# Kernel tuning notes

Hardware: AMD Instinct MI355X
Metric: run time of the kernel (lower is better)

Reference implementation:

```python
import jax, jax.numpy as jnp
import numpy as np

THRESHOLD = 10.0  # degrees, PlanetaryGraphConstruction default


def _norm_adj(lon):
    # lon: [B, P] longitudes in degrees
    diff = jnp.abs(lon[:, :, None] - lon[:, None, :]) % 360.0
    dist = jnp.minimum(diff, 360.0 - diff)            # circular angular distance, diag = 0
    mask = (dist < THRESHOLD).astype(lon.dtype)       # distance edges (diag included: 0 < 10)
    P = lon.shape[1]
    A = mask + jnp.eye(P, dtype=lon.dtype)            # GCNConv add_self_loops appends another self loop
    deg = A.sum(-1)
    dinv = jax.lax.rsqrt(jnp.maximum(deg, 1e-12))
    return A * dinv[:, :, None] * dinv[:, None, :]    # D^-1/2 (A+I) D^-1/2, [B, P, P]


def setup_inputs() -> dict:
    key = jax.random.key(0)
    ks = jax.random.split(key, 10)
    B, P, Din, H, Dout = 65536, 12, 32, 128, 3
    L = 3
    x = jax.random.uniform(ks[0], (B, P, Din), dtype=jnp.float32) * 360.0  # col 0 = longitude in degrees
    s = 0.02
    return {
        "x": x,
        "W_in": jax.random.normal(ks[1], (Din, H), jnp.float32) * s,
        "b_in": jnp.zeros((H,), jnp.float32),
        "W_gcn": jax.random.normal(ks[2], (L, H, H), jnp.float32) * s,
        "b_gcn": jnp.zeros((L, H), jnp.float32),
        "W_out1": jax.random.normal(ks[3], (H, H // 2), jnp.float32) * s,
        "b_out1": jnp.zeros((H // 2,), jnp.float32),
        "W_out2": jax.random.normal(ks[4], (H // 2, Dout), jnp.float32) * s,
        "b_out2": jnp.zeros((Dout,), jnp.float32),
    }


def reference(x, W_in, b_in, W_gcn, b_gcn, W_out1, b_out1, W_out2, b_out2):
    # x: [B, P, Din]
    Ahat = _norm_adj(x[:, :, 0])                      # [B, P, P] normalized adjacency
    h = x @ W_in + b_in                               # input projection, [B, P, H]
    for l in range(W_gcn.shape[0]):                   # GCN layers (dropout = identity in eval)
        h = jnp.einsum('bij,bjh->bih', Ahat, h @ W_gcn[l]) + b_gcn[l]
        h = jax.nn.relu(h)
    g = h.mean(axis=1)                                # mean pool over planets, [B, H]
    g = jax.nn.relu(g @ W_out1 + b_out1)
    return g @ W_out2 + b_out2                        # [B, Dout]
```

## Files before the change

kernel.cpp:

```cpp
#include <hip/hip_runtime.h>


typedef _Float16 half4v __attribute__((ext_vector_type(4)));
typedef _Float16 half8v __attribute__((ext_vector_type(8)));
typedef float    float4v __attribute__((ext_vector_type(4)));

constexpr int PP = 12, DIN = 32, H = 128, HO = 64, DOUT = 3, NL = 3;
constexpr int NB = 8;
constexpr int AP2 = 72;
constexpr int GTS = 136;

constexpr int WS_WG = 4096, WS_W1 = 53248, WS_TOT = 61440;

__global__ __launch_bounds__(256)
void prep_weights(const float* __restrict__ W_in, const float* __restrict__ W_gcn,
                  const float* __restrict__ W_out1, _Float16* __restrict__ ws)
{
    int e = blockIdx.x * 256 + threadIdx.x;
    if (e < WS_WG) {
        int n = e >> 5, k = e & 31;
        ws[e] = (_Float16)W_in[k * H + n];
    } else if (e < WS_W1) {
        int e2 = e - WS_WG;
        int l = e2 >> 14, r = e2 & 16383, n = r >> 7, k = r & 127;
        ws[e] = (_Float16)W_gcn[l * (H * H) + k * H + n];
    } else if (e < WS_TOT) {
        int e3 = e - WS_W1;
        int o = e3 >> 7, k = e3 & 127;
        ws[e] = (_Float16)W_out1[k * HO + o];
    }
}

__device__ inline half4v pk4(float a, float b, float c, float d) {
    half4v r; r[0] = (_Float16)a; r[1] = (_Float16)b; r[2] = (_Float16)c; r[3] = (_Float16)d;
    return r;
}

__global__ __launch_bounds__(256, 4)
void gnn_mfma(const float* __restrict__ x,
              const float* __restrict__ b_in,
              const float* __restrict__ b_gcn,
              const float* __restrict__ b_out1,
              const float* __restrict__ W_out2,
              const float* __restrict__ b_out2,
              const _Float16* __restrict__ ws,
              float* __restrict__ out)
{
    __shared__ __align__(16) _Float16 hf[2][12][512];
    _Float16* Am  = &hf[0][0][0];
    _Float16* gTT = &hf[0][0][0];
    float*    psf = (float*)&hf[1][0][0];

    const int tid  = threadIdx.x;
    const int lane = tid & 63, wave = tid >> 6;
    const int q = lane >> 4, qm = lane & 15;
    const int hh = lane >> 5, l32 = lane & 31;
    const int b0 = blockIdx.x * NB;
    const float* xblk = x + (size_t)b0 * (PP * DIN);
    const _Float16* WgT = ws + WS_WG;

    float lon_own = 0.f;
    if (l32 < PP) lon_own = xblk[(hh * 48 + wave * PP + l32) * DIN];
    float4 xa[3], xb[3];
    #pragma unroll
    for (int nt = 0; nt < 3; ++nt) {
        const float* p = xblk + (16 * nt + qm) * DIN + 8 * q;
        xa[nt] = *(const float4*)p;
        xb[nt] = *(const float4*)(p + 4);
    }

    {
        float lonj[PP];
        #pragma unroll
        for (int j = 0; j < PP; ++j) lonj[j] = __shfl(lon_own, j, 32);
        float deg = 1.0f;
        #pragma unroll
        for (int j = 0; j < PP; ++j) {
            float d = fabsf(lon_own - lonj[j]);
            d = fminf(d, 360.0f - d);
            deg += (d < 10.0f) ? 1.0f : 0.0f;
        }
        float dinv_own = rsqrtf(fmaxf(deg, 1e-12f));
        float dj[PP];
        #pragma unroll
        for (int j = 0; j < PP; ++j) dj[j] = __shfl(dinv_own, j, 32);

        if (l32 < PP) {
            _Float16* Ar = Am + (hh * 48 + wave * PP + l32) * AP2;
            half8v z = {0, 0, 0, 0, 0, 0, 0, 0};
            #pragma unroll
            for (int c = 0; c < 48; c += 8) *(half8v*)&Ar[c] = z;
            _Float16 vals[PP];
            #pragma unroll
            for (int j = 0; j < PP; ++j) {
                float d = fabsf(lon_own - lonj[j]);
                d = fminf(d, 360.0f - d);
                float a = (d < 10.0f) ? 1.0f : 0.0f;
                if (j == l32) a += 1.0f;
                vals[j] = (_Float16)(a * dinv_own * dj[j]);
            }
            #pragma unroll
            for (int t4 = 0; t4 < 3; ++t4) {
                half4v v;
                v[0] = vals[4 * t4]; v[1] = vals[4 * t4 + 1];
                v[2] = vals[4 * t4 + 2]; v[3] = vals[4 * t4 + 3];
                *(half4v*)&Ar[wave * PP + 4 * t4] = v;
            }
        }
    }
    __syncthreads();

    half4v bAf[2][7];
    #pragma unroll
    for (int h = 0; h < 2; ++h) {
        const _Float16* Ah = Am + h * 48 * AP2;
        bAf[h][0] = *(const half4v*)&Ah[qm * AP2 + 4 * q];
        bAf[h][1] = *(const half4v*)&Ah[qm * AP2 + 16 + 4 * q];
        bAf[h][2] = *(const half4v*)&Ah[(16 + qm) * AP2 + 4 * q];
        bAf[h][3] = *(const half4v*)&Ah[(16 + qm) * AP2 + 16 + 4 * q];
        bAf[h][4] = *(const half4v*)&Ah[(16 + qm) * AP2 + 32 + 4 * q];
        bAf[h][5] = *(const half4v*)&Ah[(32 + qm) * AP2 + 16 + 4 * q];
        bAf[h][6] = *(const half4v*)&Ah[(32 + qm) * AP2 + 32 + 4 * q];
    }
    __syncthreads();

    half8v bxA[3];
    #pragma unroll
    for (int nt = 0; nt < 3; ++nt) {
        half8v h;
        h[0] = (_Float16)xa[nt].x; h[1] = (_Float16)xa[nt].y;
        h[2] = (_Float16)xa[nt].z; h[3] = (_Float16)xa[nt].w;
        h[4] = (_Float16)xb[nt].x; h[5] = (_Float16)xb[nt].y;
        h[6] = (_Float16)xb[nt].z; h[7] = (_Float16)xb[nt].w;
        bxA[nt] = h;
    }
    #pragma unroll
    for (int nt = 0; nt < 3; ++nt) {
        const float* p = xblk + (48 + 16 * nt + qm) * DIN + 8 * q;
        xa[nt] = *(const float4*)p;
        xb[nt] = *(const float4*)(p + 4);
    }

    {
        const int m0 = 32 * wave, m1 = 32 * wave + 16;
        half8v aw0 = *(const half8v*)&ws[(m0 + qm) * DIN + 8 * q];
        half8v aw1 = *(const half8v*)&ws[(m1 + qm) * DIN + 8 * q];
        float4 bi0 = *(const float4*)&b_in[m0 + 4 * q];
        float4 bi1 = *(const float4*)&b_in[m1 + 4 * q];
        const float4v ci0 = {bi0.x, bi0.y, bi0.z, bi0.w};
        const float4v ci1 = {bi1.x, bi1.y, bi1.z, bi1.w};
        const int ho0 = (qm + 16 * ((q >> 1) & 3)) * 8 + (q & 1) * 4;
        const int ho1 = (qm + 16 * ((2 + (q >> 1)) & 3)) * 8 + (q & 1) * 4;
        #pragma unroll
        for (int nt = 0; nt < 3; ++nt) {
            float4v c0 = ci0, c1 = ci1;
            c0 = __builtin_amdgcn_mfma_f32_16x16x32_f16(aw0, bxA[nt], c0, 0, 0, 0);
            c1 = __builtin_amdgcn_mfma_f32_16x16x32_f16(aw1, bxA[nt], c1, 0, 0, 0);
            *(half4v*)&hf[0][nt * 4 + wave][ho0] = pk4(c0[0], c0[1], c0[2], c0[3]);
            *(half4v*)&hf[0][nt * 4 + wave][ho1] = pk4(c1[0], c1[1], c1[2], c1[3]);
        }
        half8v bxB[3];
        #pragma unroll
        for (int nt = 0; nt < 3; ++nt) {
            half8v h;
            h[0] = (_Float16)xa[nt].x; h[1] = (_Float16)xa[nt].y;
            h[2] = (_Float16)xa[nt].z; h[3] = (_Float16)xa[nt].w;
            h[4] = (_Float16)xb[nt].x; h[5] = (_Float16)xb[nt].y;
            h[6] = (_Float16)xb[nt].z; h[7] = (_Float16)xb[nt].w;
            bxB[nt] = h;
        }
        #pragma unroll
        for (int nt = 0; nt < 3; ++nt) {
            float4v c0 = ci0, c1 = ci1;
            c0 = __builtin_amdgcn_mfma_f32_16x16x32_f16(aw0, bxB[nt], c0, 0, 0, 0);
            c1 = __builtin_amdgcn_mfma_f32_16x16x32_f16(aw1, bxB[nt], c1, 0, 0, 0);
            *(half4v*)&hf[1][nt * 4 + wave][ho0] = pk4(c0[0], c0[1], c0[2], c0[3]);
            *(half4v*)&hf[1][nt * 4 + wave][ho1] = pk4(c1[0], c1[1], c1[2], c1[3]);
        }
    }

    half8v bw[2][4];
    #pragma unroll
    for (int n2 = 0; n2 < 2; ++n2)
        #pragma unroll
        for (int kt = 0; kt < 4; ++kt)
            bw[n2][kt] = *(const half8v*)&WgT[(32 * wave + 16 * n2 + qm) * H + 32 * kt + 8 * q];

    __syncthreads();

    #pragma unroll
    for (int l = 0; l < NL; ++l) {
        half4v ah[2][3][2];
        #pragma unroll
        for (int h = 0; h < 2; ++h) {
            float4v c[3][2];
            #pragma unroll
            for (int mt = 0; mt < 3; ++mt) {
                c[mt][0] = (float4v){0.f, 0.f, 0.f, 0.f};
                c[mt][1] = (float4v){0.f, 0.f, 0.f, 0.f};
            }
            #pragma unroll
            for (int kt = 0; kt < 4; ++kt)
                #pragma unroll
                for (int mt = 0; mt < 3; ++mt) {
                    half8v a = *(const half8v*)&hf[h][mt * 4 + kt][lane * 8];
                    c[mt][0] = __builtin_amdgcn_mfma_f32_16x16x32_f16(a, bw[0][kt], c[mt][0], 0, 0, 0);
                    c[mt][1] = __builtin_amdgcn_mfma_f32_16x16x32_f16(a, bw[1][kt], c[mt][1], 0, 0, 0);
                }
            #pragma unroll
            for (int mt = 0; mt < 3; ++mt)
                #pragma unroll
                for (int n2 = 0; n2 < 2; ++n2)
                    ah[h][mt][n2] = pk4(c[mt][n2][0], c[mt][n2][1], c[mt][n2][2], c[mt][n2][3]);
        }

        if (l < 2) {
            const float4 bg0 = *(const float4*)&b_gcn[l * H + 32 * wave + 4 * q];
            const float4 bg1 = *(const float4*)&b_gcn[l * H + 32 * wave + 16 + 4 * q];
            __syncthreads();

            {
                const _Float16* Wn = WgT + (l + 1) * (H * H);
                #pragma unroll
                for (int n2 = 0; n2 < 2; ++n2)
                    #pragma unroll
                    for (int kt = 0; kt < 4; ++kt)
                        bw[n2][kt] = *(const half8v*)&Wn[(32 * wave + 16 * n2 + qm) * H + 32 * kt + 8 * q];
            }

            #pragma unroll
            for (int h = 0; h < 2; ++h) {
                #pragma unroll
                for (int n2 = 0; n2 < 2; ++n2) {
                    const float4 bg = n2 ? bg1 : bg0;
                    const float4v di = {bg.x, bg.y, bg.z, bg.w};
                    const int hoff = (qm + 16 * ((2 * n2 + (q >> 1)) & 3)) * 8 + (q & 1) * 4;

                    float4v d0 = di;
                    d0 = __builtin_amdgcn_mfma_f32_16x16x16f16(ah[h][0][n2], bAf[h][0], d0, 0, 0, 0);
                    d0 = __builtin_amdgcn_mfma_f32_16x16x16f16(ah[h][1][n2], bAf[h][1], d0, 0, 0, 0);
                    *(half4v*)&hf[h][0 * 4 + wave][hoff] =
                        pk4(fmaxf(d0[0], 0.f), fmaxf(d0[1], 0.f),
                            fmaxf(d0[2], 0.f), fmaxf(d0[3], 0.f));

                    float4v d1 = di;
                    d1 = __builtin_amdgcn_mfma_f32_16x16x16f16(ah[h][0][n2], bAf[h][2], d1, 0, 0, 0);
                    d1 = __builtin_amdgcn_mfma_f32_16x16x16f16(ah[h][1][n2], bAf[h][3], d1, 0, 0, 0);
                    d1 = __builtin_amdgcn_mfma_f32_16x16x16f16(ah[h][2][n2], bAf[h][4], d1, 0, 0, 0);
                    *(half4v*)&hf[h][1 * 4 + wave][hoff] =
                        pk4(fmaxf(d1[0], 0.f), fmaxf(d1[1], 0.f),
                            fmaxf(d1[2], 0.f), fmaxf(d1[3], 0.f));

                    float4v d2 = di;
                    d2 = __builtin_amdgcn_mfma_f32_16x16x16f16(ah[h][1][n2], bAf[h][5], d2, 0, 0, 0);
                    d2 = __builtin_amdgcn_mfma_f32_16x16x16f16(ah[h][2][n2], bAf[h][6], d2, 0, 0, 0);
                    *(half4v*)&hf[h][2 * 4 + wave][hoff] =
                        pk4(fmaxf(d2[0], 0.f), fmaxf(d2[1], 0.f),
                            fmaxf(d2[2], 0.f), fmaxf(d2[3], 0.f));
                }
            }
            __syncthreads();
        } else {
            __syncthreads();
            const float bgc0 = b_gcn[2 * H + 32 * wave + qm];
            const float bgc1 = b_gcn[2 * H + 32 * wave + 16 + qm];
            #pragma unroll
            for (int h = 0; h < 2; ++h) {
                float s[3][2];
                #pragma unroll
                for (int n2 = 0; n2 < 2; ++n2) {
                    const float bgc = n2 ? bgc1 : bgc0;
                    const float4v di = {bgc, bgc, bgc, bgc};
                    float4v d;
                    d = di;
                    d = __builtin_amdgcn_mfma_f32_16x16x16f16(bAf[h][0], ah[h][0][n2], d, 0, 0, 0);
                    d = __builtin_amdgcn_mfma_f32_16x16x16f16(bAf[h][1], ah[h][1][n2], d, 0, 0, 0);
                    s[0][n2] = fmaxf(d[0], 0.f) + fmaxf(d[1], 0.f)
                             + fmaxf(d[2], 0.f) + fmaxf(d[3], 0.f);
                    d = di;
                    d = __builtin_amdgcn_mfma_f32_16x16x16f16(bAf[h][2], ah[h][0][n2], d, 0, 0, 0);
                    d = __builtin_amdgcn_mfma_f32_16x16x16f16(bAf[h][3], ah[h][1][n2], d, 0, 0, 0);
                    d = __builtin_amdgcn_mfma_f32_16x16x16f16(bAf[h][4], ah[h][2][n2], d, 0, 0, 0);
                    s[1][n2] = fmaxf(d[0], 0.f) + fmaxf(d[1], 0.f)
                             + fmaxf(d[2], 0.f) + fmaxf(d[3], 0.f);
                    d = di;
                    d = __builtin_amdgcn_mfma_f32_16x16x16f16(bAf[h][5], ah[h][1][n2], d, 0, 0, 0);
                    d = __builtin_amdgcn_mfma_f32_16x16x16f16(bAf[h][6], ah[h][2][n2], d, 0, 0, 0);
                    s[2][n2] = fmaxf(d[0], 0.f) + fmaxf(d[1], 0.f)
                             + fmaxf(d[2], 0.f) + fmaxf(d[3], 0.f);
                }
                #pragma unroll
                for (int n2 = 0; n2 < 2; ++n2) {
                    float g4[4];
                    g4[0] = (q <= 2) ? s[0][n2] : 0.f;
                    g4[1] = (q == 3) ? s[0][n2] : ((q <= 1) ? s[1][n2] : 0.f);
                    g4[2] = (q >= 2) ? s[1][n2] : ((q == 0) ? s[2][n2] : 0.f);
                    g4[3] = (q >= 1) ? s[2][n2] : 0.f;
                    #pragma unroll
                    for (int b = 0; b < 4; ++b) {
                        float v = g4[b];
                        v += __shfl_xor(v, 16, 64);
                        v += __shfl_xor(v, 32, 64);
                        if (q == 0)
                            gTT[(4 * h + b) * GTS + 32 * wave + 16 * n2 + qm] =
                                (_Float16)(v * (1.0f / 12.0f));
                    }
                }
            }
            __syncthreads();
        }
    }

    const float4 b1v = *(const float4*)&b_out1[16 * wave + 4 * q];
    float4v acc = {b1v.x, b1v.y, b1v.z, b1v.w};
    #pragma unroll
    for (int kt = 0; kt < 4; ++kt) {
        half8v aW = *(const half8v*)&ws[WS_W1 + (16 * wave + qm) * H + 32 * kt + 8 * q];
        half8v bG = *(const half8v*)&gTT[qm * GTS + 32 * kt + 8 * q];
        acc = __builtin_amdgcn_mfma_f32_16x16x32_f16(aW, bG, acc, 0, 0, 0);
    }
    float o1v[4];
    o1v[0] = fmaxf(acc[0], 0.f);
    o1v[1] = fmaxf(acc[1], 0.f);
    o1v[2] = fmaxf(acc[2], 0.f);
    o1v[3] = fmaxf(acc[3], 0.f);
    const float* w2p = W_out2 + (16 * wave + 4 * q) * DOUT;
    const float4 w2a = *(const float4*)(w2p);
    const float4 w2b = *(const float4*)(w2p + 4);
    const float4 w2c = *(const float4*)(w2p + 8);
    float p0 = o1v[0] * w2a.x + o1v[1] * w2a.w + o1v[2] * w2b.z + o1v[3] * w2c.y;
    float p1 = o1v[0] * w2a.y + o1v[1] * w2b.x + o1v[2] * w2b.w + o1v[3] * w2c.z;
    float p2 = o1v[0] * w2a.z + o1v[1] * w2b.y + o1v[2] * w2c.x + o1v[3] * w2c.w;
    p0 += __shfl_xor(p0, 16, 64); p0 += __shfl_xor(p0, 32, 64);
    p1 += __shfl_xor(p1, 16, 64); p1 += __shfl_xor(p1, 32, 64);
    p2 += __shfl_xor(p2, 16, 64); p2 += __shfl_xor(p2, 32, 64);
    if (q == 0 && qm < NB) {
        psf[wave * (NB * DOUT) + qm * DOUT + 0] = p0;
        psf[wave * (NB * DOUT) + qm * DOUT + 1] = p1;
        psf[wave * (NB * DOUT) + qm * DOUT + 2] = p2;
    }
    __syncthreads();
    if (tid < NB * DOUT) {
        const int b = tid / 3, d = tid - 3 * b;
        const float ssum = psf[b * 3 + d] + psf[24 + b * 3 + d]
                         + psf[48 + b * 3 + d] + psf[72 + b * 3 + d] + b_out2[d];
        out[(size_t)(b0 + b) * DOUT + d] = ssum;
    }
}

extern "C" void kernel_launch(void* const* d_in, const int* in_sizes, int n_in,
                              void* d_out, int out_size, void* d_ws, size_t ws_size,
                              hipStream_t stream) {
    const float* x      = (const float*)d_in[0];
    const float* W_in   = (const float*)d_in[1];
    const float* b_in   = (const float*)d_in[2];
    const float* W_gcn  = (const float*)d_in[3];
    const float* b_gcn  = (const float*)d_in[4];
    const float* W_out1 = (const float*)d_in[5];
    const float* b_out1 = (const float*)d_in[6];
    const float* W_out2 = (const float*)d_in[7];
    const float* b_out2 = (const float*)d_in[8];
    float* outp         = (float*)d_out;
    _Float16* wsh       = (_Float16*)d_ws;

    const int B = in_sizes[0] / (PP * DIN);

    hipLaunchKernelGGL(prep_weights, dim3((WS_TOT + 255) / 256), dim3(256), 0, stream,
                       W_in, W_gcn, W_out1, wsh);
    hipLaunchKernelGGL(gnn_mfma, dim3(B / NB), dim3(256), 0, stream,
                       x, b_in, b_gcn, b_out1, W_out2, b_out2, wsh, outp);
}
```

Measured before the change: 296.8 us.

## Split each block's two 4-sample halves across 8 waves instead of 4

Doubles the block to 512 threads so waves 4-7 process the second half of the 8 samples in parallel, instead of each wave looping over both halves sequentially. Each wave now keeps only one half's adjacency fragments and activations, which cuts per-thread register state. The intent is more parallelism and latency hiding per block. The cost is that the bw weight fragments are duplicated across the two wave groups, waves 4-7 sit idle during adjacency build and the output head, and the launch-bounds change alters occupancy.

```diff
diff --git a/kernel.cpp b/kernel.cpp
--- a/kernel.cpp
+++ b/kernel.cpp
@@ -36,7 +36,7 @@
     return r;
 }
 
-__global__ __launch_bounds__(256, 4)
+__global__ __launch_bounds__(512, 4)
 void gnn_mfma(const float* __restrict__ x,
               const float* __restrict__ b_in,
               const float* __restrict__ b_gcn,
@@ -53,23 +53,24 @@
 
     const int tid  = threadIdx.x;
     const int lane = tid & 63, wave = tid >> 6;
+    const int hfsel = wave >> 2, w4 = wave & 3;
     const int q = lane >> 4, qm = lane & 15;
     const int hh = lane >> 5, l32 = lane & 31;
     const int b0 = blockIdx.x * NB;
     const float* xblk = x + (size_t)b0 * (PP * DIN);
     const _Float16* WgT = ws + WS_WG;
 
-    float lon_own = 0.f;
-    if (l32 < PP) lon_own = xblk[(hh * 48 + wave * PP + l32) * DIN];
     float4 xa[3], xb[3];
     #pragma unroll
     for (int nt = 0; nt < 3; ++nt) {
-        const float* p = xblk + (16 * nt + qm) * DIN + 8 * q;
+        const float* p = xblk + (hfsel * 48 + 16 * nt + qm) * DIN + 8 * q;
         xa[nt] = *(const float4*)p;
         xb[nt] = *(const float4*)(p + 4);
     }
 
-    {
+    if (wave < 4) {
+        float lon_own = 0.f;
+        if (l32 < PP) lon_own = xblk[(hh * 48 + wave * PP + l32) * DIN];
         float lonj[PP];
         #pragma unroll
         for (int j = 0; j < PP; ++j) lonj[j] = __shfl(lon_own, j, 32);
@@ -110,21 +111,20 @@
     }
     __syncthreads();
 
-    half4v bAf[2][7];
-    #pragma unroll
-    for (int h = 0; h < 2; ++h) {
-        const _Float16* Ah = Am + h * 48 * AP2;
-        bAf[h][0] = *(const half4v*)&Ah[qm * AP2 + 4 * q];
-        bAf[h][1] = *(const half4v*)&Ah[qm * AP2 + 16 + 4 * q];
-        bAf[h][2] = *(const half4v*)&Ah[(16 + qm) * AP2 + 4 * q];
-        bAf[h][3] = *(const half4v*)&Ah[(16 + qm) * AP2 + 16 + 4 * q];
-        bAf[h][4] = *(const half4v*)&Ah[(16 + qm) * AP2 + 32 + 4 * q];
-        bAf[h][5] = *(const half4v*)&Ah[(32 + qm) * AP2 + 16 + 4 * q];
-        bAf[h][6] = *(const half4v*)&Ah[(32 + qm) * AP2 + 32 + 4 * q];
+    half4v bAf[7];
+    {
+        const _Float16* Ah = Am + hfsel * 48 * AP2;
+        bAf[0] = *(const half4v*)&Ah[qm * AP2 + 4 * q];
+        bAf[1] = *(const half4v*)&Ah[qm * AP2 + 16 + 4 * q];
+        bAf[2] = *(const half4v*)&Ah[(16 + qm) * AP2 + 4 * q];
+        bAf[3] = *(const half4v*)&Ah[(16 + qm) * AP2 + 16 + 4 * q];
+        bAf[4] = *(const half4v*)&Ah[(16 + qm) * AP2 + 32 + 4 * q];
+        bAf[5] = *(const half4v*)&Ah[(32 + qm) * AP2 + 16 + 4 * q];
+        bAf[6] = *(const half4v*)&Ah[(32 + qm) * AP2 + 32 + 4 * q];
     }
     __syncthreads();
 
-    half8v bxA[3];
+    half8v bx[3];
     #pragma unroll
     for (int nt = 0; nt < 3; ++nt) {
         half8v h;
@@ -132,17 +132,11 @@
         h[2] = (_Float16)xa[nt].z; h[3] = (_Float16)xa[nt].w;
         h[4] = (_Float16)xb[nt].x; h[5] = (_Float16)xb[nt].y;
         h[6] = (_Float16)xb[nt].z; h[7] = (_Float16)xb[nt].w;
-        bxA[nt] = h;
-    }
-    #pragma unroll
-    for (int nt = 0; nt < 3; ++nt) {
-        const float* p = xblk + (48 + 16 * nt + qm) * DIN + 8 * q;
-        xa[nt] = *(const float4*)p;
-        xb[nt] = *(const float4*)(p + 4);
+        bx[nt] = h;
     }
 
     {
-        const int m0 = 32 * wave, m1 = 32 * wave + 16;
+        const int m0 = 32 * w4, m1 = 32 * w4 + 16;
         half8v aw0 = *(const half8v*)&ws[(m0 + qm) * DIN + 8 * q];
         half8v aw1 = *(const half8v*)&ws[(m1 + qm) * DIN + 8 * q];
         float4 bi0 = *(const float4*)&b_in[m0 + 4 * q];
@@ -154,28 +148,10 @@
         #pragma unroll
         for (int nt = 0; nt < 3; ++nt) {
             float4v c0 = ci0, c1 = ci1;
-            c0 = __builtin_amdgcn_mfma_f32_16x16x32_f16(aw0, bxA[nt], c0, 0, 0, 0);
-            c1 = __builtin_amdgcn_mfma_f32_16x16x32_f16(aw1, bxA[nt], c1, 0, 0, 0);
-            *(half4v*)&hf[0][nt * 4 + wave][ho0] = pk4(c0[0], c0[1], c0[2], c0[3]);
-            *(half4v*)&hf[0][nt * 4 + wave][ho1] = pk4(c1[0], c1[1], c1[2], c1[3]);
-        }
-        half8v bxB[3];
-        #pragma unroll
-        for (int nt = 0; nt < 3; ++nt) {
-            half8v h;
-            h[0] = (_Float16)xa[nt].x; h[1] = (_Float16)xa[nt].y;
-            h[2] = (_Float16)xa[nt].z; h[3] = (_Float16)xa[nt].w;
-            h[4] = (_Float16)xb[nt].x; h[5] = (_Float16)xb[nt].y;
-            h[6] = (_Float16)xb[nt].z; h[7] = (_Float16)xb[nt].w;
-            bxB[nt] = h;
-        }
-        #pragma unroll
-        for (int nt = 0; nt < 3; ++nt) {
-            float4v c0 = ci0, c1 = ci1;
-            c0 = __builtin_amdgcn_mfma_f32_16x16x32_f16(aw0, bxB[nt], c0, 0, 0, 0);
-            c1 = __builtin_amdgcn_mfma_f32_16x16x32_f16(aw1, bxB[nt], c1, 0, 0, 0);
-            *(half4v*)&hf[1][nt * 4 + wave][ho0] = pk4(c0[0], c0[1], c0[2], c0[3]);
-            *(half4v*)&hf[1][nt * 4 + wave][ho1] = pk4(c1[0], c1[1], c1[2], c1[3]);
+            c0 = __builtin_amdgcn_mfma_f32_16x16x32_f16(aw0, bx[nt], c0, 0, 0, 0);
+            c1 = __builtin_amdgcn_mfma_f32_16x16x32_f16(aw1, bx[nt], c1, 0, 0, 0);
+            *(half4v*)&hf[hfsel][nt * 4 + w4][ho0] = pk4(c0[0], c0[1], c0[2], c0[3]);
+            *(half4v*)&hf[hfsel][nt * 4 + w4][ho1] = pk4(c1[0], c1[1], c1[2], c1[3]);
         }
     }
 
@@ -184,15 +160,14 @@
     for (int n2 = 0; n2 < 2; ++n2)
         #pragma unroll
         for (int kt = 0; kt < 4; ++kt)
-            bw[n2][kt] = *(const half8v*)&WgT[(32 * wave + 16 * n2 + qm) * H + 32 * kt + 8 * q];
+            bw[n2][kt] = *(const half8v*)&WgT[(32 * w4 + 16 * n2 + qm) * H + 32 * kt + 8 * q];
 
     __syncthreads();
 
     #pragma unroll
     for (int l = 0; l < NL; ++l) {
-        half4v ah[2][3][2];
-        #pragma unroll
-        for (int h = 0; h < 2; ++h) {
+        half4v ah[3][2];
+        {
             float4v c[3][2];
             #pragma unroll
             for (int mt = 0; mt < 3; ++mt) {
@@ -203,7 +178,7 @@
             for (int kt = 0; kt < 4; ++kt)
                 #pragma unroll
                 for (int mt = 0; mt < 3; ++mt) {
-                    half8v a = *(const half8v*)&hf[h][mt * 4 + kt][lane * 8];
+                    half8v a = *(const half8v*)&hf[hfsel][mt * 4 + kt][lane * 8];
                     c[mt][0] = __builtin_amdgcn_mfma_f32_16x16x32_f16(a, bw[0][kt], c[mt][0], 0, 0, 0);
                     c[mt][1] = __builtin_amdgcn_mfma_f32_16x16x32_f16(a, bw[1][kt], c[mt][1], 0, 0, 0);
                 }
@@ -211,12 +186,12 @@
             for (int mt = 0; mt < 3; ++mt)
                 #pragma unroll
                 for (int n2 = 0; n2 < 2; ++n2)
-                    ah[h][mt][n2] = pk4(c[mt][n2][0], c[mt][n2][1], c[mt][n2][2], c[mt][n2][3]);
+                    ah[mt][n2] = pk4(c[mt][n2][0], c[mt][n2][1], c[mt][n2][2], c[mt][n2][3]);
         }
 
         if (l < 2) {
-            const float4 bg0 = *(const float4*)&b_gcn[l * H + 32 * wave + 4 * q];
-            const float4 bg1 = *(const float4*)&b_gcn[l * H + 32 * wave + 16 + 4 * q];
+            const float4 bg0 = *(const float4*)&b_gcn[l * H + 32 * w4 + 4 * q];
+            const float4 bg1 = *(const float4*)&b_gcn[l * H + 32 * w4 + 16 + 4 * q];
             __syncthreads();
 
             {
@@ -225,119 +200,115 @@
                 for (int n2 = 0; n2 < 2; ++n2)
                     #pragma unroll
                     for (int kt = 0; kt < 4; ++kt)
-                        bw[n2][kt] = *(const half8v*)&Wn[(32 * wave + 16 * n2 + qm) * H + 32 * kt + 8 * q];
-            }
-
-            #pragma unroll
-            for (int h = 0; h < 2; ++h) {
-                #pragma unroll
-                for (int n2 = 0; n2 < 2; ++n2) {
-                    const float4 bg = n2 ? bg1 : bg0;
-                    const float4v di = {bg.x, bg.y, bg.z, bg.w};
-                    const int hoff = (qm + 16 * ((2 * n2 + (q >> 1)) & 3)) * 8 + (q & 1) * 4;
-
-                    float4v d0 = di;
-                    d0 = __builtin_amdgcn_mfma_f32_16x16x16f16(ah[h][0][n2], bAf[h][0], d0, 0, 0, 0);
-                    d0 = __builtin_amdgcn_mfma_f32_16x16x16f16(ah[h][1][n2], bAf[h][1], d0, 0, 0, 0);
-                    *(half4v*)&hf[h][0 * 4 + wave][hoff] =
-                        pk4(fmaxf(d0[0], 0.f), fmaxf(d0[1], 0.f),
-                            fmaxf(d0[2], 0.f), fmaxf(d0[3], 0.f));
-
-                    float4v d1 = di;
-                    d1 = __builtin_amdgcn_mfma_f32_16x16x16f16(ah[h][0][n2], bAf[h][2], d1, 0, 0, 0);
-                    d1 = __builtin_amdgcn_mfma_f32_16x16x16f16(ah[h][1][n2], bAf[h][3], d1, 0, 0, 0);
-                    d1 = __builtin_amdgcn_mfma_f32_16x16x16f16(ah[h][2][n2], bAf[h][4], d1, 0, 0, 0);
-                    *(half4v*)&hf[h][1 * 4 + wave][hoff] =
-                        pk4(fmaxf(d1[0], 0.f), fmaxf(d1[1], 0.f),
-                            fmaxf(d1[2], 0.f), fmaxf(d1[3], 0.f));
-
-                    float4v d2 = di;
-                    d2 = __builtin_amdgcn_mfma_f32_16x16x16f16(ah[h][1][n2], bAf[h][5], d2, 0, 0, 0);
-                    d2 = __builtin_amdgcn_mfma_f32_16x16x16f16(ah[h][2][n2], bAf[h][6], d2, 0, 0, 0);
-                    *(half4v*)&hf[h][2 * 4 + wave][hoff] =
-                        pk4(fmaxf(d2[0], 0.f), fmaxf(d2[1], 0.f),
-                            fmaxf(d2[2], 0.f), fmaxf(d2[3], 0.f));
-                }
+                        bw[n2][kt] = *(const half8v*)&Wn[(32 * w4 + 16 * n2 + qm) * H + 32 * kt + 8 * q];
+            }
+
+            #pragma unroll
+            for (int n2 = 0; n2 < 2; ++n2) {
+                const float4 bg = n2 ? bg1 : bg0;
+                const float4v di = {bg.x, bg.y, bg.z, bg.w};
+                const int hoff = (qm + 16 * ((2 * n2 + (q >> 1)) & 3)) * 8 + (q & 1) * 4;
+
+                float4v d0 = di;
+                d0 = __builtin_amdgcn_mfma_f32_16x16x16f16(ah[0][n2], bAf[0], d0, 0, 0, 0);
+                d0 = __builtin_amdgcn_mfma_f32_16x16x16f16(ah[1][n2], bAf[1], d0, 0, 0, 0);
+                *(half4v*)&hf[hfsel][0 * 4 + w4][hoff] =
+                    pk4(fmaxf(d0[0], 0.f), fmaxf(d0[1], 0.f),
+                        fmaxf(d0[2], 0.f), fmaxf(d0[3], 0.f));
+
+                float4v d1 = di;
+                d1 = __builtin_amdgcn_mfma_f32_16x16x16f16(ah[0][n2], bAf[2], d1, 0, 0, 0);
+                d1 = __builtin_amdgcn_mfma_f32_16x16x16f16(ah[1][n2], bAf[3], d1, 0, 0, 0);
+                d1 = __builtin_amdgcn_mfma_f32_16x16x16f16(ah[2][n2], bAf[4], d1, 0, 0, 0);
+                *(half4v*)&hf[hfsel][1 * 4 + w4][hoff] =
+                    pk4(fmaxf(d1[0], 0.f), fmaxf(d1[1], 0.f),
+                        fmaxf(d1[2], 0.f), fmaxf(d1[3], 0.f));
+
+                float4v d2 = di;
+                d2 = __builtin_amdgcn_mfma_f32_16x16x16f16(ah[1][n2], bAf[5], d2, 0, 0, 0);
+                d2 = __builtin_amdgcn_mfma_f32_16x16x16f16(ah[2][n2], bAf[6], d2, 0, 0, 0);
+                *(half4v*)&hf[hfsel][2 * 4 + w4][hoff] =
+                    pk4(fmaxf(d2[0], 0.f), fmaxf(d2[1], 0.f),
+                        fmaxf(d2[2], 0.f), fmaxf(d2[3], 0.f));
             }
             __syncthreads();
         } else {
             __syncthreads();
-            const float bgc0 = b_gcn[2 * H + 32 * wave + qm];
-            const float bgc1 = b_gcn[2 * H + 32 * wave + 16 + qm];
-            #pragma unroll
-            for (int h = 0; h < 2; ++h) {
-                float s[3][2];
+            const float bgc0 = b_gcn[2 * H + 32 * w4 + qm];
+            const float bgc1 = b_gcn[2 * H + 32 * w4 + 16 + qm];
+            float s[3][2];
+            #pragma unroll
+            for (int n2 = 0; n2 < 2; ++n2) {
+                const float bgc = n2 ? bgc1 : bgc0;
+                const float4v di = {bgc, bgc, bgc, bgc};
+                float4v d;
+                d = di;
+                d = __builtin_amdgcn_mfma_f32_16x16x16f16(bAf[0], ah[0][n2], d, 0, 0, 0);
+                d = __builtin_amdgcn_mfma_f32_16x16x16f16(bAf[1], ah[1][n2], d, 0, 0, 0);
+                s[0][n2] = fmaxf(d[0], 0.f) + fmaxf(d[1], 0.f)
+                         + fmaxf(d[2], 0.f) + fmaxf(d[3], 0.f);
+                d = di;
+                d = __builtin_amdgcn_mfma_f32_16x16x16f16(bAf[2], ah[0][n2], d, 0, 0, 0);
+                d = __builtin_amdgcn_mfma_f32_16x16x16f16(bAf[3], ah[1][n2], d, 0, 0, 0);
+                d = __builtin_amdgcn_mfma_f32_16x16x16f16(bAf[4], ah[2][n2], d, 0, 0, 0);
+                s[1][n2] = fmaxf(d[0], 0.f) + fmaxf(d[1], 0.f)
+                         + fmaxf(d[2], 0.f) + fmaxf(d[3], 0.f);
+                d = di;
+                d = __builtin_amdgcn_mfma_f32_16x16x16f16(bAf[5], ah[1][n2], d, 0, 0, 0);
+                d = __builtin_amdgcn_mfma_f32_16x16x16f16(bAf[6], ah[2][n2], d, 0, 0, 0);
+                s[2][n2] = fmaxf(d[0], 0.f) + fmaxf(d[1], 0.f)
+                         + fmaxf(d[2], 0.f) + fmaxf(d[3], 0.f);
+            }
+            #pragma unroll
+            for (int n2 = 0; n2 < 2; ++n2) {
+                float g4[4];
+                g4[0] = (q <= 2) ? s[0][n2] : 0.f;
+                g4[1] = (q == 3) ? s[0][n2] : ((q <= 1) ? s[1][n2] : 0.f);
+                g4[2] = (q >= 2) ? s[1][n2] : ((q == 0) ? s[2][n2] : 0.f);
+                g4[3] = (q >= 1) ? s[2][n2] : 0.f;
                 #pragma unroll
-                for (int n2 = 0; n2 < 2; ++n2) {
-                    const float bgc = n2 ? bgc1 : bgc0;
-                    const float4v di = {bgc, bgc, bgc, bgc};
-                    float4v d;
-                    d = di;
-                    d = __builtin_amdgcn_mfma_f32_16x16x16f16(bAf[h][0], ah[h][0][n2], d, 0, 0, 0);
-                    d = __builtin_amdgcn_mfma_f32_16x16x16f16(bAf[h][1], ah[h][1][n2], d, 0, 0, 0);
-                    s[0][n2] = fmaxf(d[0], 0.f) + fmaxf(d[1], 0.f)
-                             + fmaxf(d[2], 0.f) + fmaxf(d[3], 0.f);
-                    d = di;
-                    d = __builtin_amdgcn_mfma_f32_16x16x16f16(bAf[h][2], ah[h][0][n2], d, 0, 0, 0);
-                    d = __builtin_amdgcn_mfma_f32_16x16x16f16(bAf[h][3], ah[h][1][n2], d, 0, 0, 0);
-                    d = __builtin_amdgcn_mfma_f32_16x16x16f16(bAf[h][4], ah[h][2][n2], d, 0, 0, 0);
-                    s[1][n2] = fmaxf(d[0], 0.f) + fmaxf(d[1], 0.f)
-                             + fmaxf(d[2], 0.f) + fmaxf(d[3], 0.f);
-                    d = di;
-                    d = __builtin_amdgcn_mfma_f32_16x16x16f16(bAf[h][5], ah[h][1][n2], d, 0, 0, 0);
-                    d = __builtin_amdgcn_mfma_f32_16x16x16f16(bAf[h][6], ah[h][2][n2], d, 0, 0, 0);
-                    s[2][n2] = fmaxf(d[0], 0.f) + fmaxf(d[1], 0.f)
-                             + fmaxf(d[2], 0.f) + fmaxf(d[3], 0.f);
+                for (int b = 0; b < 4; ++b) {
+                    float v = g4[b];
+                    v += __shfl_xor(v, 16, 64);
+                    v += __shfl_xor(v, 32, 64);
+                    if (q == 0)
+                        gTT[(4 * hfsel + b) * GTS + 32 * w4 + 16 * n2 + qm] =
+                            (_Float16)(v * (1.0f / 12.0f));
                 }
-                #pragma unroll
-                for (int n2 = 0; n2 < 2; ++n2) {
-                    float g4[4];
-                    g4[0] = (q <= 2) ? s[0][n2] : 0.f;
-                    g4[1] = (q == 3) ? s[0][n2] : ((q <= 1) ? s[1][n2] : 0.f);
-                    g4[2] = (q >= 2) ? s[1][n2] : ((q == 0) ? s[2][n2] : 0.f);
-                    g4[3] = (q >= 1) ? s[2][n2] : 0.f;
-                    #pragma unroll
-                    for (int b = 0; b < 4; ++b) {
-                        float v = g4[b];
-                        v += __shfl_xor(v, 16, 64);
-                        v += __shfl_xor(v, 32, 64);
-                        if (q == 0)
-                            gTT[(4 * h + b) * GTS + 32 * wave + 16 * n2 + qm] =
-                                (_Float16)(v * (1.0f / 12.0f));
-                    }
-                }
             }
             __syncthreads();
         }
     }
 
-    const float4 b1v = *(const float4*)&b_out1[16 * wave + 4 * q];
-    float4v acc = {b1v.x, b1v.y, b1v.z, b1v.w};
-    #pragma unroll
-    for (int kt = 0; kt < 4; ++kt) {
-        half8v aW = *(const half8v*)&ws[WS_W1 + (16 * wave + qm) * H + 32 * kt + 8 * q];
-        half8v bG = *(const half8v*)&gTT[qm * GTS + 32 * kt + 8 * q];
-        acc = __builtin_amdgcn_mfma_f32_16x16x32_f16(aW, bG, acc, 0, 0, 0);
-    }
-    float o1v[4];
-    o1v[0] = fmaxf(acc[0], 0.f);
-    o1v[1] = fmaxf(acc[1], 0.f);
-    o1v[2] = fmaxf(acc[2], 0.f);
-    o1v[3] = fmaxf(acc[3], 0.f);
-    const float* w2p = W_out2 + (16 * wave + 4 * q) * DOUT;
-    const float4 w2a = *(const float4*)(w2p);
-    const float4 w2b = *(const float4*)(w2p + 4);
-    const float4 w2c = *(const float4*)(w2p + 8);
-    float p0 = o1v[0] * w2a.x + o1v[1] * w2a.w + o1v[2] * w2b.z + o1v[3] * w2c.y;
-    float p1 = o1v[0] * w2a.y + o1v[1] * w2b.x + o1v[2] * w2b.w + o1v[3] * w2c.z;
-    float p2 = o1v[0] * w2a.z + o1v[1] * w2b.y + o1v[2] * w2c.x + o1v[3] * w2c.w;
-    p0 += __shfl_xor(p0, 16, 64); p0 += __shfl_xor(p0, 32, 64);
-    p1 += __shfl_xor(p1, 16, 64); p1 += __shfl_xor(p1, 32, 64);
-    p2 += __shfl_xor(p2, 16, 64); p2 += __shfl_xor(p2, 32, 64);
-    if (q == 0 && qm < NB) {
-        psf[wave * (NB * DOUT) + qm * DOUT + 0] = p0;
-        psf[wave * (NB * DOUT) + qm * DOUT + 1] = p1;
-        psf[wave * (NB * DOUT) + qm * DOUT + 2] = p2;
+    if (wave < 4) {
+        const float4 b1v = *(const float4*)&b_out1[16 * wave + 4 * q];
+        float4v acc = {b1v.x, b1v.y, b1v.z, b1v.w};
+        #pragma unroll
+        for (int kt = 0; kt < 4; ++kt) {
+            half8v aW = *(const half8v*)&ws[WS_W1 + (16 * wave + qm) * H + 32 * kt + 8 * q];
+            half8v bG = *(const half8v*)&gTT[qm * GTS + 32 * kt + 8 * q];
+            acc = __builtin_amdgcn_mfma_f32_16x16x32_f16(aW, bG, acc, 0, 0, 0);
+        }
+        float o1v[4];
+        o1v[0] = fmaxf(acc[0], 0.f);
+        o1v[1] = fmaxf(acc[1], 0.f);
+        o1v[2] = fmaxf(acc[2], 0.f);
+        o1v[3] = fmaxf(acc[3], 0.f);
+        const float* w2p = W_out2 + (16 * wave + 4 * q) * DOUT;
+        const float4 w2a = *(const float4*)(w2p);
+        const float4 w2b = *(const float4*)(w2p + 4);
+        const float4 w2c = *(const float4*)(w2p + 8);
+        float p0 = o1v[0] * w2a.x + o1v[1] * w2a.w + o1v[2] * w2b.z + o1v[3] * w2c.y;
+        float p1 = o1v[0] * w2a.y + o1v[1] * w2b.x + o1v[2] * w2b.w + o1v[3] * w2c.z;
+        float p2 = o1v[0] * w2a.z + o1v[1] * w2b.y + o1v[2] * w2c.x + o1v[3] * w2c.w;
+        p0 += __shfl_xor(p0, 16, 64); p0 += __shfl_xor(p0, 32, 64);
+        p1 += __shfl_xor(p1, 16, 64); p1 += __shfl_xor(p1, 32, 64);
+        p2 += __shfl_xor(p2, 16, 64); p2 += __shfl_xor(p2, 32, 64);
+        if (q == 0 && qm < NB) {
+            psf[wave * (NB * DOUT) + qm * DOUT + 0] = p0;
+            psf[wave * (NB * DOUT) + qm * DOUT + 1] = p1;
+            psf[wave * (NB * DOUT) + qm * DOUT + 2] = p2;
+        }
     }
     __syncthreads();
     if (tid < NB * DOUT) {
@@ -367,6 +338,6 @@
 
     hipLaunchKernelGGL(prep_weights, dim3((WS_TOT + 255) / 256), dim3(256), 0, stream,
                        W_in, W_gcn, W_out1, wsh);
-    hipLaunchKernelGGL(gnn_mfma, dim3(B / NB), dim3(256), 0, stream,
+    hipLaunchKernelGGL(gnn_mfma, dim3(B / NB), dim3(512), 0, stream,
                        x, b_in, b_gcn, b_out1, W_out2, b_out2, wsh, outp);
 }
```

After: 405.6 us. +36.6%, slower.
